# Optimization experiments

Hardware: AMD Instinct MI355X
Metric: run time of the kernel (lower is better)

The kernel has to match this reference:

```python
import jax, jax.numpy as jnp
import numpy as np

R0 = 1.0
N_NODES = 10000
N_EDGES = 160000
DIM_A, DIM_V, DIM_D, CHAN = 64, 32, 16, 16

# Levi-Civita tensor for the antisymmetric (cross-product-like) products
_EPS = np.zeros((3, 3, 3), dtype=np.float32)
for (i, j, k), s in (((0,1,2),1.),((1,2,0),1.),((2,0,1),1.),((0,2,1),-1.),((2,1,0),-1.),((1,0,2),-1.)):
    _EPS[i, j, k] = s


def _tl(W, x):
    """TensLinear: mix channel axis 1 of x (B, din, *(3,)*rank) with W (dout, din)."""
    y = jnp.tensordot(x, W, axes=((1,), (1,)))  # (B, *(3,)*rank, dout)
    return jnp.moveaxis(y, -1, 1)


def radial_encode_8(r, r0):
    # 8 Gaussian radial basis functions on |r|/r0
    d = jnp.linalg.norm(r, axis=-1)            # (E,)
    x = d * (8.0 / r0)
    mu = jnp.arange(8, dtype=r.dtype)
    return jnp.exp(-0.5 * (x[:, None] - mu[None, :]) ** 2)  # (E, 8)


def tens_sigmoid_1(v):
    # equivariant squashing: scale vector by tanh(|v|)/|v|
    n = jnp.linalg.norm(v, axis=-1, keepdims=True)
    return v * jnp.tanh(n) / (n + 1e-12)


def _forward(floats, src, dst, n_nodes):
    (r_ij, x_a, x_v, x_d, W_L0, W_L1, W_L2,
     W_Y000, W_Y110, W_Y220, W_Y011, W_Y101, W_Y121, W_Y211,
     W_Y022, W_Y202, W_Y112, W_Y222, W_Y111, W_Y212,
     W_enc, b_enc, W_dir, W1, b1, W2, b2, W3, b3) = floats
    eps = jnp.asarray(_EPS)
    rad = radial_encode_8(r_ij, R0) @ W_enc.T + b_enc        # (E, chan)
    r = tens_sigmoid_1(r_ij * (7.0 / R0))                    # (E, 3)
    phi_a = rad                                              # (E, chan)
    phi_v = rad[:, :, None] * r[:, None, :]                  # (E, chan, 3)
    phi_d = rad[:, :, None, None] * r[:, None, None, :] * r[:, None, :, None]  # (E, chan, 3, 3)
    # gather destination-node features per edge
    x_a_j = _tl(W_L0, x_a)[dst]                              # (E, chan)
    x_v_j = _tl(W_L1, x_v)[dst]                              # (E, chan, 3)
    x_d_j = _tl(W_L2, x_d)[dst]                              # (E, chan, 3, 3)
    # equivariant tensor products (Bee.apply)
    y_000 = x_a_j * phi_a
    y_110 = jnp.sum(x_v_j * phi_v, -1)
    y_220 = jnp.sum(x_d_j * phi_d, (-2, -1))
    y_011 = x_a_j[..., None] * phi_v
    y_101 = x_v_j * phi_a[..., None]
    y_121 = jnp.einsum('ecj,ecji->eci', x_v_j, phi_d)
    y_211 = jnp.einsum('ecij,ecj->eci', x_d_j, phi_v)
    y_022 = x_a_j[..., None, None] * phi_d
    y_202 = x_d_j * phi_a[..., None, None]
    y_112 = x_v_j[..., :, None] * phi_v[..., None, :]
    y_222 = jnp.einsum('ecik,eckj->ecij', x_d_j, phi_d)
    y_111 = jnp.cross(x_v_j, phi_v)
    y_212 = jnp.einsum('ikl,eckj,ecl->ecij', eps, x_d_j, phi_v)
    psi_a = _tl(W_Y000, y_000) + _tl(W_Y110, y_110) + _tl(W_Y220, y_220)
    psi_v = (_tl(W_Y011, y_011) + _tl(W_Y101, y_101) + _tl(W_Y121, y_121)
             + _tl(W_Y211, y_211) + _tl(W_Y111, y_111))
    psi_d = (_tl(W_Y022, y_022) + _tl(W_Y202, y_202) + _tl(W_Y112, y_112)
             + _tl(W_Y222, y_222) + _tl(W_Y212, y_212))
    # residual MLP on the scalar channel: lin_direct(x) + layers(x)
    lrelu = lambda x: jnp.where(x >= 0, x, 0.1 * x)
    h = lrelu(psi_a @ W1.T + b1)
    h = lrelu(h @ W2.T + b2)
    psi_a = psi_a + psi_a @ W_dir.T + (h @ W3.T + b3)
    # scatter-reduce messages to source nodes
    B_a = jax.ops.segment_sum(psi_a, src, num_segments=n_nodes)
    B_v = jax.ops.segment_sum(psi_v, src, num_segments=n_nodes)
    B_d = jax.ops.segment_sum(psi_d, src, num_segments=n_nodes)
    return 0.1 * B_a, 0.1 * B_v, 0.1 * B_d


def setup_inputs() -> dict:
    key = jax.random.key(0)
    ks = jax.random.split(key, 32)
    f32 = jnp.float32
    nrm = lambda k, shape, scale=1.0: scale * jax.random.normal(k, shape, dtype=f32)
    E, N = N_EDGES, N_NODES
    sC = CHAN ** -0.5
    inp = {
        'r_ij': nrm(ks[0], (E, 3)),
        'x_a': nrm(ks[1], (N, DIM_A)),
        'x_v': nrm(ks[2], (N, DIM_V, 3)),
        'x_d': nrm(ks[3], (N, DIM_D, 3, 3)),
        'W_L0': nrm(ks[4], (CHAN, DIM_A), DIM_A ** -0.5),
        'W_L1': nrm(ks[5], (CHAN, DIM_V), DIM_V ** -0.5),
        'W_L2': nrm(ks[6], (CHAN, DIM_D), DIM_D ** -0.5),
        'W_Y000': nrm(ks[7], (DIM_A, CHAN), sC),
        'W_Y110': nrm(ks[8], (DIM_A, CHAN), sC),
        'W_Y220': nrm(ks[9], (DIM_A, CHAN), sC),
        'W_Y011': nrm(ks[10], (DIM_V, CHAN), sC),
        'W_Y101': nrm(ks[11], (DIM_V, CHAN), sC),
        'W_Y121': nrm(ks[12], (DIM_V, CHAN), sC),
        'W_Y211': nrm(ks[13], (DIM_V, CHAN), sC),
        'W_Y022': nrm(ks[14], (DIM_D, CHAN), sC),
        'W_Y202': nrm(ks[15], (DIM_D, CHAN), sC),
        'W_Y112': nrm(ks[16], (DIM_D, CHAN), sC),
        'W_Y222': nrm(ks[17], (DIM_D, CHAN), sC),
        'W_Y111': nrm(ks[18], (DIM_V, CHAN), sC),
        'W_Y212': nrm(ks[19], (DIM_D, CHAN), sC),
        'W_enc': nrm(ks[20], (CHAN, 8), 8 ** -0.5),
        'b_enc': jnp.zeros((CHAN,), f32),
        'W_dir': nrm(ks[21], (DIM_A, DIM_A), DIM_A ** -0.5),
        'W1': nrm(ks[22], (2 * DIM_A, DIM_A), DIM_A ** -0.5),
        'b1': jnp.zeros((2 * DIM_A,), f32),
        'W2': nrm(ks[23], (2 * DIM_A, 2 * DIM_A), (2 * DIM_A) ** -0.5),
        'b2': jnp.zeros((2 * DIM_A,), f32),
        'W3': nrm(ks[24], (DIM_A, 2 * DIM_A), (2 * DIM_A) ** -0.5),
        'b3': jnp.zeros((DIM_A,), f32),
        'src': jax.random.randint(ks[25], (E,), 0, N, dtype=jnp.int32),
        'dst': jax.random.randint(ks[26], (E,), 0, N, dtype=jnp.int32),
        'n_nodes': N,
    }
    return inp


def reference(r_ij, x_a, x_v, x_d, W_L0, W_L1, W_L2, W_Y000, W_Y110, W_Y220,
              W_Y011, W_Y101, W_Y121, W_Y211, W_Y022, W_Y202, W_Y112, W_Y222,
              W_Y111, W_Y212, W_enc, b_enc, W_dir, W1, b1, W2, b2, W3, b3,
              src, dst, n_nodes):
    floats = (r_ij, x_a, x_v, x_d, W_L0, W_L1, W_L2, W_Y000, W_Y110, W_Y220,
              W_Y011, W_Y101, W_Y121, W_Y211, W_Y022, W_Y202, W_Y112, W_Y222,
              W_Y111, W_Y212, W_enc, b_enc, W_dir, W1, b1, W2, b2, W3, b3)
    return _forward(floats, src, dst, n_nodes)
```

## Files before the change

### kernel.cpp

```cpp
#include <hip/hip_runtime.h>
#include <hip/hip_bf16.h>

typedef __hip_bfloat16 bf16;
typedef __attribute__((ext_vector_type(8))) short bf16x8;
typedef __attribute__((ext_vector_type(4))) float f32x4;

__device__ __forceinline__ void st_bf16(short* p, float v) {
    uint32_t u = __float_as_uint(v) + 0x8000u;
    *p = (short)(u >> 16);
}
__device__ __forceinline__ float bb2f(short s) {
    uint32_t u = ((uint32_t)(uint16_t)s) << 16;
    return __uint_as_float(u);
}

__global__ void zero_i32(int* p, int n) {
    int i = blockIdx.x * blockDim.x + threadIdx.x;
    int stride = gridDim.x * blockDim.x;
    for (; i < n; i += stride) p[i] = 0;
}

__global__ __launch_bounds__(256) void prep_all(
    const float* __restrict__ W000, const float* __restrict__ W110, const float* __restrict__ W220,
    const float* __restrict__ W011, const float* __restrict__ W101, const float* __restrict__ W121,
    const float* __restrict__ W211, const float* __restrict__ W111,
    const float* __restrict__ W022, const float* __restrict__ W202, const float* __restrict__ W112,
    const float* __restrict__ W222, const float* __restrict__ W212,
    const float* __restrict__ W1, const float* __restrict__ W2, const float* __restrict__ W3,
    const float* __restrict__ Wdir, bf16* __restrict__ wout,
    const float* __restrict__ xa, const float* __restrict__ xv, const float* __restrict__ xd,
    const float* __restrict__ WL0, const float* __restrict__ WL1, const float* __restrict__ WL2,
    float* __restrict__ Pa, float* __restrict__ Pv, float* __restrict__ Pd, int N, int NPB,
    const int* __restrict__ src, int* __restrict__ cnt, int E)
{
    int b = blockIdx.x;
    const int tid = threadIdx.x;
    if (b < 178) {
        int i = b * 256 + tid;
        if (i >= 45568) return;
        float v = 0.f;
        if (i < 4096) {
            int o = i >> 6, k = i & 63;
            if (k < 48) {
                int t = k >> 4, c = k & 15;
                const float* W = (t == 0) ? W000 : (t == 1) ? W110 : W220;
                v = W[o * 16 + c];
            }
        } else if (i < 7168) {
            int r = i - 4096, ch = r / 96, k = r % 96;
            if (k < 80) {
                int t = k >> 4, c = k & 15;
                const float* W = (t == 0) ? W011 : (t == 1) ? W101 : (t == 2) ? W121 : (t == 3) ? W211 : W111;
                v = W[ch * 16 + c];
            }
        } else if (i < 8704) {
            int r = i - 7168, ch = r / 96, k = r % 96;
            if (k < 80) {
                int t = k >> 4, c = k & 15;
                const float* W = (t == 0) ? W022 : (t == 1) ? W202 : (t == 2) ? W112 : (t == 3) ? W222 : W212;
                v = W[ch * 16 + c];
            }
        } else if (i < 16896) v = W1[i - 8704];
        else if (i < 33280) v = W2[i - 16896];
        else if (i < 41472) v = W3[i - 33280];
        else v = Wdir[i - 41472];
        wout[i] = __float2bfloat16(v);
        return;
    }
    b -= 178;
    if (b < NPB) {
        __shared__ float sxa[256], sxv[384], sxd[576];
        const int n0 = b * 4;
        if (n0 + tid / 64 < N) sxa[tid] = xa[(size_t)n0 * 64 + tid];
        for (int i = tid; i < 384; i += 256) if (n0 + i / 96 < N)  sxv[i] = xv[(size_t)n0 * 96 + i];
        for (int i = tid; i < 576; i += 256) if (n0 + i / 144 < N) sxd[i] = xd[(size_t)n0 * 144 + i];
        __syncthreads();
        for (int o = tid; o < 832; o += 256) {
            int ln = o / 208, s = o % 208;
            int n = n0 + ln;
            if (n >= N) continue;
            if (s < 16) {
                float a = 0.f;
                const float* w = WL0 + s * 64;
                const float* x = sxa + ln * 64;
                for (int d = 0; d < 64; ++d) a += w[d] * x[d];
                Pa[(size_t)n * 16 + s] = a;
            } else if (s < 64) {
                int idx = s - 16, c = idx / 3, i = idx % 3;
                float a = 0.f;
                const float* w = WL1 + c * 32;
                const float* x = sxv + ln * 96;
                for (int d = 0; d < 32; ++d) a += w[d] * x[d * 3 + i];
                Pv[(size_t)n * 64 + c * 4 + i] = a;
            } else {
                int idx = s - 64, c = idx / 9, ij = idx % 9;
                float a = 0.f;
                const float* w = WL2 + c * 16;
                const float* x = sxd + ln * 144;
                for (int d = 0; d < 16; ++d) a += w[d] * x[d * 9 + ij];
                Pd[(size_t)n * 192 + c * 12 + ij] = a;
            }
        }
        return;
    }
    b -= NPB;
    int i = b * 256 + tid;
    if (i < E) atomicAdd(&cnt[src[i]], 1);
}

__global__ void scan_rows(const int* __restrict__ cnt, int* __restrict__ rowstart, int N) {
    __shared__ int ps[256];
    int t = threadIdx.x;
    int chunk = (N + 255) / 256;
    int base = t * chunk;
    int s = 0;
    for (int i = 0; i < chunk; ++i) { int idx = base + i; if (idx < N) s += cnt[idx]; }
    ps[t] = s;
    __syncthreads();
    for (int off = 1; off < 256; off <<= 1) {
        int v = (t >= off) ? ps[t - off] : 0;
        __syncthreads();
        ps[t] += v;
        __syncthreads();
    }
    int run = (t > 0) ? ps[t - 1] : 0;
    for (int i = 0; i < chunk; ++i) {
        int idx = base + i;
        if (idx < N) { rowstart[idx] = run; run += cnt[idx]; }
    }
    if (t == 255) rowstart[N] = run;
}

__global__ void fill_slot(const int* __restrict__ src, const int* __restrict__ rowstart,
                          int* __restrict__ cursor, int* __restrict__ slot, int E) {
    int i = blockIdx.x * 256 + threadIdx.x;
    if (i < E) slot[i] = rowstart[src[i]] + atomicAdd(&cursor[src[i]], 1);
}

__global__ __launch_bounds__(256) void edge_mfma(
    const float* __restrict__ r_ij,
    const float* __restrict__ Pa, const float* __restrict__ Pv, const float* __restrict__ Pd,
    const float* __restrict__ Wenc, const float* __restrict__ benc,
    const bf16* __restrict__ Wa, const bf16* __restrict__ Wv, const bf16* __restrict__ Wd,
    const bf16* __restrict__ Wb1, const bf16* __restrict__ Wb2,
    const bf16* __restrict__ Wb3, const bf16* __restrict__ Wbdir,
    const float* __restrict__ b1, const float* __restrict__ b2, const float* __restrict__ b3,
    const int* __restrict__ slot, const int* __restrict__ dst,
    short* __restrict__ psi, int E)
{
    __shared__ __align__(16) char smem[32320];
    short* SYA   = (short*)smem;
    short* SYV   = (short*)(smem + 1536);
    short* SYD   = (short*)(smem + 9216);
    int*   SSLOT = (int*)(smem + 32256);
    short* SPSIA = (short*)(smem + 1536);
    short* SH1   = (short*)(smem + 3840);
    short* SH2   = (short*)(smem + 8192);
    short* SPSI  = (short*)(smem + 12544);

    const int tid = threadIdx.x;
    const int e0 = blockIdx.x * 16;
    const bf16x8 z8 = {};

    {
        const int le = tid >> 4, c = tid & 15;
        const int e = e0 + le;
        if (e < E) {
            const int j = dst[e];
            if (c == 0) SSLOT[le] = slot[e];
            float vx = 7.f * r_ij[e * 3 + 0];
            float vy = 7.f * r_ij[e * 3 + 1];
            float vz = 7.f * r_ij[e * 3 + 2];
            float nn = sqrtf(vx * vx + vy * vy + vz * vz);
            float ex = __expf(-2.f * nn);
            float th = (1.f - ex) * __builtin_amdgcn_rcpf(1.f + ex);
            float sc = th * __builtin_amdgcn_rcpf(nn + 1e-12f);
            float rr[3] = {vx * sc, vy * sc, vz * sc};
            float x8 = nn * (8.f / 7.f);
            float rad = benc[c];
            #pragma unroll
            for (int m = 0; m < 8; ++m) {
                float tt = x8 - (float)m;
                rad += __expf(-0.5f * tt * tt) * Wenc[c * 8 + m];
            }
            float xa = Pa[j * 16 + c];
            f32x4 pv4 = *(const f32x4*)(Pv + (size_t)j * 64 + c * 4);
            f32x4 pd0 = *(const f32x4*)(Pd + (size_t)j * 192 + c * 12);
            f32x4 pd1 = *(const f32x4*)(Pd + (size_t)j * 192 + c * 12 + 4);
            f32x4 pd2 = *(const f32x4*)(Pd + (size_t)j * 192 + c * 12 + 8);
            float xv[3] = {pv4[0], pv4[1], pv4[2]};
            float xd[9] = {pd0[0], pd0[1], pd0[2], pd0[3], pd1[0], pd1[1], pd1[2], pd1[3], pd2[0]};
            float dotv = xv[0] * rr[0] + xv[1] * rr[1] + xv[2] * rr[2];
            float mv[3];
            #pragma unroll
            for (int i = 0; i < 3; ++i)
                mv[i] = xd[i * 3] * rr[0] + xd[i * 3 + 1] * rr[1] + xd[i * 3 + 2] * rr[2];
            float quad = mv[0] * rr[0] + mv[1] * rr[1] + mv[2] * rr[2];
            st_bf16(&SYA[le * 48 + c],      xa * rad);
            st_bf16(&SYA[le * 48 + 16 + c], rad * dotv);
            st_bf16(&SYA[le * 48 + 32 + c], rad * quad);
            #pragma unroll
            for (int i = 0; i < 3; ++i) {
                int row = (le * 3 + i) * 80;
                int i1 = (i + 1) % 3, i2 = (i + 2) % 3;
                st_bf16(&SYV[row + c],      xa * rad * rr[i]);
                st_bf16(&SYV[row + 16 + c], rad * xv[i]);
                st_bf16(&SYV[row + 32 + c], rad * dotv * rr[i]);
                st_bf16(&SYV[row + 48 + c], rad * mv[i]);
                st_bf16(&SYV[row + 64 + c], rad * (xv[i1] * rr[i2] - xv[i2] * rr[i1]));
            }
            #pragma unroll
            for (int i = 0; i < 3; ++i) {
                int i1 = (i + 1) % 3, i2 = (i + 2) % 3;
                #pragma unroll
                for (int jj = 0; jj < 3; ++jj) {
                    int row = (le * 9 + i * 3 + jj) * 80;
                    st_bf16(&SYD[row + c],      xa * rad * rr[i] * rr[jj]);
                    st_bf16(&SYD[row + 16 + c], rad * xd[i * 3 + jj]);
                    st_bf16(&SYD[row + 32 + c], rad * xv[i] * rr[jj]);
                    st_bf16(&SYD[row + 48 + c], rad * mv[i] * rr[jj]);
                    st_bf16(&SYD[row + 64 + c], rad * (xd[i1 * 3 + jj] * rr[i2] - xd[i2 * 3 + jj] * rr[i1]));
                }
            }
        }
    }
    __syncthreads();

    const int wid = tid >> 6, lane = tid & 63;
    const int q = lane >> 4, r16 = lane & 15;

    f32x4 da[4] = {};
    f32x4 dv[3][2] = {};
    f32x4 dd[5] = {};
    const int mstart = (wid == 2) ? 0 : 5;
    const int mcnt = (wid == 2) ? 5 : 4;

    if (wid == 0) {
        bf16x8 af0 = *(const bf16x8*)&SYA[r16 * 48 + q * 8];
        bf16x8 af1 = z8;
        if (q < 2) af1 = *(const bf16x8*)&SYA[r16 * 48 + 32 + q * 8];
        #pragma unroll
        for (int n = 0; n < 4; ++n) {
            bf16x8 bf0 = *(const bf16x8*)((const short*)Wa + (n * 16 + r16) * 64 + q * 8);
            bf16x8 bf1 = *(const bf16x8*)((const short*)Wa + (n * 16 + r16) * 64 + 32 + q * 8);
            da[n] = __builtin_amdgcn_mfma_f32_16x16x32_bf16(af0, bf0, da[n], 0, 0, 0);
            da[n] = __builtin_amdgcn_mfma_f32_16x16x32_bf16(af1, bf1, da[n], 0, 0, 0);
        }
    } else if (wid == 1) {
        #pragma unroll
        for (int ks = 0; ks < 3; ++ks) {
            bf16x8 av[3], bv[2];
            #pragma unroll
            for (int m = 0; m < 3; ++m) {
                if (ks < 2) av[m] = *(const bf16x8*)&SYV[(m * 16 + r16) * 80 + ks * 32 + q * 8];
                else {
                    av[m] = z8;
                    if (q < 2) av[m] = *(const bf16x8*)&SYV[(m * 16 + r16) * 80 + 64 + q * 8];
                }
            }
            #pragma unroll
            for (int n = 0; n < 2; ++n)
                bv[n] = *(const bf16x8*)((const short*)Wv + (n * 16 + r16) * 96 + ks * 32 + q * 8);
            #pragma unroll
            for (int m = 0; m < 3; ++m)
                #pragma unroll
                for (int n = 0; n < 2; ++n)
                    dv[m][n] = __builtin_amdgcn_mfma_f32_16x16x32_bf16(av[m], bv[n], dv[m][n], 0, 0, 0);
        }
    } else {
        #pragma unroll
        for (int ks = 0; ks < 3; ++ks) {
            bf16x8 bf = *(const bf16x8*)((const short*)Wd + r16 * 96 + ks * 32 + q * 8);
            for (int mi = 0; mi < mcnt; ++mi) {
                bf16x8 af;
                if (ks < 2) af = *(const bf16x8*)&SYD[((mstart + mi) * 16 + r16) * 80 + ks * 32 + q * 8];
                else {
                    af = z8;
                    if (q < 2) af = *(const bf16x8*)&SYD[((mstart + mi) * 16 + r16) * 80 + 64 + q * 8];
                }
                dd[mi] = __builtin_amdgcn_mfma_f32_16x16x32_bf16(af, bf, dd[mi], 0, 0, 0);
            }
        }
    }
    __syncthreads();

    if (wid == 0) {
        #pragma unroll
        for (int n = 0; n < 4; ++n)
            #pragma unroll
            for (int jj = 0; jj < 4; ++jj)
                st_bf16(&SPSIA[(q * 4 + jj) * 72 + n * 16 + r16], da[n][jj]);
    } else if (wid == 1) {
        #pragma unroll
        for (int m = 0; m < 3; ++m)
            #pragma unroll
            for (int n = 0; n < 2; ++n)
                #pragma unroll
                for (int jj = 0; jj < 4; ++jj) {
                    int row = m * 16 + q * 4 + jj;
                    int el = row / 3, i = row % 3;
                    st_bf16(&SPSI[el * 304 + 64 + (n * 16 + r16) * 3 + i], dv[m][n][jj]);
                }
    } else {
        for (int mi = 0; mi < mcnt; ++mi)
            #pragma unroll
            for (int jj = 0; jj < 4; ++jj) {
                int row = (mstart + mi) * 16 + q * 4 + jj;
                int el = row / 9, ij = row % 9;
                st_bf16(&SPSI[el * 304 + 160 + r16 * 9 + ij], dd[mi][jj]);
            }
    }
    __syncthreads();

    {
        f32x4 h1a[2] = {};
        #pragma unroll
        for (int ks = 0; ks < 2; ++ks) {
            bf16x8 af = *(const bf16x8*)&SPSIA[r16 * 72 + ks * 32 + q * 8];
            #pragma unroll
            for (int n = 0; n < 2; ++n) {
                int col = wid * 32 + n * 16 + r16;
                bf16x8 bf = *(const bf16x8*)((const short*)Wb1 + col * 64 + ks * 32 + q * 8);
                h1a[n] = __builtin_amdgcn_mfma_f32_16x16x32_bf16(af, bf, h1a[n], 0, 0, 0);
            }
        }
        #pragma unroll
        for (int n = 0; n < 2; ++n) {
            int col = wid * 32 + n * 16 + r16;
            float bias = b1[col];
            #pragma unroll
            for (int jj = 0; jj < 4; ++jj) {
                float v = h1a[n][jj] + bias;
                v = v >= 0.f ? v : 0.1f * v;
                st_bf16(&SH1[(q * 4 + jj) * 136 + col], v);
            }
        }
    }
    __syncthreads();
    {
        f32x4 h2a[2] = {};
        #pragma unroll
        for (int ks = 0; ks < 4; ++ks) {
            bf16x8 af = *(const bf16x8*)&SH1[r16 * 136 + ks * 32 + q * 8];
            #pragma unroll
            for (int n = 0; n < 2; ++n) {
                int col = wid * 32 + n * 16 + r16;
                bf16x8 bf = *(const bf16x8*)((const short*)Wb2 + col * 128 + ks * 32 + q * 8);
                h2a[n] = __builtin_amdgcn_mfma_f32_16x16x32_bf16(af, bf, h2a[n], 0, 0, 0);
            }
        }
        #pragma unroll
        for (int n = 0; n < 2; ++n) {
            int col = wid * 32 + n * 16 + r16;
            float bias = b2[col];
            #pragma unroll
            for (int jj = 0; jj < 4; ++jj) {
                float v = h2a[n][jj] + bias;
                v = v >= 0.f ? v : 0.1f * v;
                st_bf16(&SH2[(q * 4 + jj) * 136 + col], v);
            }
        }
    }
    __syncthreads();
    {
        f32x4 o3 = {};
        const int col3 = wid * 16 + r16;
        #pragma unroll
        for (int ks = 0; ks < 4; ++ks) {
            bf16x8 af = *(const bf16x8*)&SH2[r16 * 136 + ks * 32 + q * 8];
            bf16x8 bf = *(const bf16x8*)((const short*)Wb3 + col3 * 128 + ks * 32 + q * 8);
            o3 = __builtin_amdgcn_mfma_f32_16x16x32_bf16(af, bf, o3, 0, 0, 0);
        }
        #pragma unroll
        for (int ks = 0; ks < 2; ++ks) {
            bf16x8 af = *(const bf16x8*)&SPSIA[r16 * 72 + ks * 32 + q * 8];
            bf16x8 bf = *(const bf16x8*)((const short*)Wbdir + col3 * 64 + ks * 32 + q * 8);
            o3 = __builtin_amdgcn_mfma_f32_16x16x32_bf16(af, bf, o3, 0, 0, 0);
        }
        float bias = b3[col3];
        #pragma unroll
        for (int jj = 0; jj < 4; ++jj) {
            int row = q * 4 + jj;
            float v = o3[jj] + bias + bb2f(SPSIA[row * 72 + col3]);
            st_bf16(&SPSI[row * 304 + col3], v);
        }
    }
    __syncthreads();

    {
        const uint32_t* S32 = (const uint32_t*)SPSI;
        uint32_t* P32 = (uint32_t*)psi;
        for (int idx = tid; idx < 16 * 152; idx += 256) {
            int le = idx / 152, k = idx - le * 152;
            if (e0 + le < E)
                P32[(size_t)SSLOT[le] * 152 + k] = S32[le * 152 + k];
        }
    }
}

__global__ __launch_bounds__(192) void gather(
    const short* __restrict__ psi, const int* __restrict__ rowstart,
    float* __restrict__ out, int N) {
    int n = blockIdx.x, t = threadIdx.x;
    if (t >= 152) return;
    int s0 = rowstart[n], s1 = rowstart[n + 1];
    const uint32_t* p32 = (const uint32_t*)psi;
    float a0 = 0.f, a1 = 0.f;
    for (int s = s0; s < s1; ++s) {
        uint32_t u = p32[(size_t)s * 152 + t];
        a0 += __uint_as_float(u << 16);
        a1 += __uint_as_float(u & 0xffff0000u);
    }
    int f = 2 * t;
    float2 v = make_float2(0.1f * a0, 0.1f * a1);
    if (f < 64)       *(float2*)&out[(size_t)n * 64 + f] = v;
    else if (f < 160) *(float2*)&out[(size_t)N * 64 + (size_t)n * 96 + (f - 64)] = v;
    else              *(float2*)&out[(size_t)N * 160 + (size_t)n * 144 + (f - 160)] = v;
}

extern "C" void kernel_launch(void* const* d_in, const int* in_sizes, int n_in,
                              void* d_out, int out_size, void* d_ws, size_t ws_size,
                              hipStream_t stream) {
    const float* r_ij = (const float*)d_in[0];
    const float* x_a  = (const float*)d_in[1];
    const float* x_v  = (const float*)d_in[2];
    const float* x_d  = (const float*)d_in[3];
    const float* W_L0 = (const float*)d_in[4];
    const float* W_L1 = (const float*)d_in[5];
    const float* W_L2 = (const float*)d_in[6];
    const float* W000 = (const float*)d_in[7];
    const float* W110 = (const float*)d_in[8];
    const float* W220 = (const float*)d_in[9];
    const float* W011 = (const float*)d_in[10];
    const float* W101 = (const float*)d_in[11];
    const float* W121 = (const float*)d_in[12];
    const float* W211 = (const float*)d_in[13];
    const float* W022 = (const float*)d_in[14];
    const float* W202 = (const float*)d_in[15];
    const float* W112 = (const float*)d_in[16];
    const float* W222 = (const float*)d_in[17];
    const float* W111 = (const float*)d_in[18];
    const float* W212 = (const float*)d_in[19];
    const float* Wenc = (const float*)d_in[20];
    const float* benc = (const float*)d_in[21];
    const float* Wdir = (const float*)d_in[22];
    const float* W1   = (const float*)d_in[23];
    const float* b1   = (const float*)d_in[24];
    const float* W2   = (const float*)d_in[25];
    const float* b2   = (const float*)d_in[26];
    const float* W3   = (const float*)d_in[27];
    const float* b3   = (const float*)d_in[28];
    const int* src    = (const int*)d_in[29];
    const int* dst    = (const int*)d_in[30];

    const int E = in_sizes[29];
    const int N = in_sizes[1] / 64;

    float* Pa     = (float*)d_ws;
    float* Pv     = Pa + (size_t)N * 16;
    float* Pd     = Pv + (size_t)N * 64;
    bf16*  Wb     = (bf16*)(Pd + (size_t)N * 192);
    int*   cnt    = (int*)(Wb + 45568);
    int*   cursor = cnt + N;
    int*   rowst  = cursor + N;
    int*   slot   = rowst + N + 1;
    short* psi    = (short*)(slot + E);

    const bf16* Wa_p    = Wb;
    const bf16* Wv_p    = Wb + 4096;
    const bf16* Wd_p    = Wb + 7168;
    const bf16* Wb1_p   = Wb + 8704;
    const bf16* Wb2_p   = Wb + 16896;
    const bf16* Wb3_p   = Wb + 33280;
    const bf16* Wbdir_p = Wb + 41472;

    const int NPB = (N + 3) / 4;
    const int HB  = (E + 255) / 256;

    zero_i32<<<80, 256, 0, stream>>>(cnt, 2 * N);
    prep_all<<<178 + NPB + HB, 256, 0, stream>>>(
        W000, W110, W220, W011, W101, W121, W211, W111,
        W022, W202, W112, W222, W212, W1, W2, W3, Wdir, Wb,
        x_a, x_v, x_d, W_L0, W_L1, W_L2, Pa, Pv, Pd, N, NPB,
        src, cnt, E);
    scan_rows<<<1, 256, 0, stream>>>(cnt, rowst, N);
    fill_slot<<<HB, 256, 0, stream>>>(src, rowst, cursor, slot, E);
    edge_mfma<<<(E + 15) / 16, 256, 0, stream>>>(
        r_ij, Pa, Pv, Pd, Wenc, benc,
        Wa_p, Wv_p, Wd_p, Wb1_p, Wb2_p, Wb3_p, Wbdir_p,
        b1, b2, b3, slot, dst, psi, E);
    gather<<<N, 192, 0, stream>>>(psi, rowst, (float*)d_out, N);
}
```

Baseline: 242.1 us.

## Sort edges by destination with XCD-aware tile mapping for cache locality

Builds a second CSR keyed on dst and processes edges in dst-sorted order in edge_mfma, so that gathered node features (Pa/Pv/Pd) are reused by neighbouring edges. The block index is remapped so each XCD handles a contiguous run of tiles, which keeps the reused node data in that XCD's L2. The gather kernel now reads two words per thread with 128-thread blocks, and the zero kernel is replaced by a memset. The cost is extra atomics, a second scan and an indirection load through eperm.

```diff
diff --git a/kernel.cpp b/kernel.cpp
--- a/kernel.cpp
+++ b/kernel.cpp
@@ -12,12 +12,6 @@
 __device__ __forceinline__ float bb2f(short s) {
     uint32_t u = ((uint32_t)(uint16_t)s) << 16;
     return __uint_as_float(u);
-}
-
-__global__ void zero_i32(int* p, int n) {
-    int i = blockIdx.x * blockDim.x + threadIdx.x;
-    int stride = gridDim.x * blockDim.x;
-    for (; i < n; i += stride) p[i] = 0;
 }
 
 __global__ __launch_bounds__(256) void prep_all(
@@ -31,7 +25,8 @@
     const float* __restrict__ xa, const float* __restrict__ xv, const float* __restrict__ xd,
     const float* __restrict__ WL0, const float* __restrict__ WL1, const float* __restrict__ WL2,
     float* __restrict__ Pa, float* __restrict__ Pv, float* __restrict__ Pd, int N, int NPB,
-    const int* __restrict__ src, int* __restrict__ cnt, int E)
+    const int* __restrict__ src, const int* __restrict__ dst,
+    int* __restrict__ cnt_s, int* __restrict__ cnt_d, int E)
 {
     int b = blockIdx.x;
     const int tid = threadIdx.x;
@@ -105,10 +100,16 @@
     }
     b -= NPB;
     int i = b * 256 + tid;
-    if (i < E) atomicAdd(&cnt[src[i]], 1);
-}
-
-__global__ void scan_rows(const int* __restrict__ cnt, int* __restrict__ rowstart, int N) {
+    if (i < E) {
+        atomicAdd(&cnt_s[src[i]], 1);
+        atomicAdd(&cnt_d[dst[i]], 1);
+    }
+}
+
+__global__ void scan_rows2(const int* __restrict__ cnt_s, int* __restrict__ rs_s,
+                           const int* __restrict__ cnt_d, int* __restrict__ rs_d, int N) {
+    const int* cnt = blockIdx.x ? cnt_d : cnt_s;
+    int* rowstart = blockIdx.x ? rs_d : rs_s;
     __shared__ int ps[256];
     int t = threadIdx.x;
     int chunk = (N + 255) / 256;
@@ -131,10 +132,16 @@
     if (t == 255) rowstart[N] = run;
 }
 
-__global__ void fill_slot(const int* __restrict__ src, const int* __restrict__ rowstart,
-                          int* __restrict__ cursor, int* __restrict__ slot, int E) {
+__global__ void fill_slot(const int* __restrict__ src, const int* __restrict__ dst,
+                          const int* __restrict__ rs_s, const int* __restrict__ rs_d,
+                          int* __restrict__ cur_s, int* __restrict__ cur_d,
+                          int* __restrict__ slot, int* __restrict__ eperm, int E) {
     int i = blockIdx.x * 256 + threadIdx.x;
-    if (i < E) slot[i] = rowstart[src[i]] + atomicAdd(&cursor[src[i]], 1);
+    if (i < E) {
+        slot[i] = rs_s[src[i]] + atomicAdd(&cur_s[src[i]], 1);
+        int p = rs_d[dst[i]] + atomicAdd(&cur_d[dst[i]], 1);
+        eperm[p] = i;
+    }
 }
 
 __global__ __launch_bounds__(256) void edge_mfma(
@@ -146,7 +153,8 @@
     const bf16* __restrict__ Wb3, const bf16* __restrict__ Wbdir,
     const float* __restrict__ b1, const float* __restrict__ b2, const float* __restrict__ b3,
     const int* __restrict__ slot, const int* __restrict__ dst,
-    short* __restrict__ psi, int E)
+    const int* __restrict__ eperm,
+    short* __restrict__ psi, int E, int nwg)
 {
     __shared__ __align__(16) char smem[32320];
     short* SYA   = (short*)smem;
@@ -159,13 +167,17 @@
     short* SPSI  = (short*)(smem + 12544);
 
     const int tid = threadIdx.x;
-    const int e0 = blockIdx.x * 16;
+    int orig = blockIdx.x;
+    int q = nwg >> 3, r = nwg & 7;
+    int xcd = orig & 7, idx = orig >> 3;
+    int tile = (xcd < r) ? (xcd * (q + 1) + idx) : (r * (q + 1) + (xcd - r) * q + idx);
+    const int e0 = tile * 16;
     const bf16x8 z8 = {};
 
     {
         const int le = tid >> 4, c = tid & 15;
-        const int e = e0 + le;
-        if (e < E) {
+        if (e0 + le < E) {
+            const int e = eperm[e0 + le];
             const int j = dst[e];
             if (c == 0) SSLOT[le] = slot[e];
             float vx = 7.f * r_ij[e * 3 + 0];
@@ -227,7 +239,7 @@
     __syncthreads();
 
     const int wid = tid >> 6, lane = tid & 63;
-    const int q = lane >> 4, r16 = lane & 15;
+    const int q16 = lane >> 4, r16 = lane & 15;
 
     f32x4 da[4] = {};
     f32x4 dv[3][2] = {};
@@ -236,13 +248,13 @@
     const int mcnt = (wid == 2) ? 5 : 4;
 
     if (wid == 0) {
-        bf16x8 af0 = *(const bf16x8*)&SYA[r16 * 48 + q * 8];
+        bf16x8 af0 = *(const bf16x8*)&SYA[r16 * 48 + q16 * 8];
         bf16x8 af1 = z8;
-        if (q < 2) af1 = *(const bf16x8*)&SYA[r16 * 48 + 32 + q * 8];
+        if (q16 < 2) af1 = *(const bf16x8*)&SYA[r16 * 48 + 32 + q16 * 8];
         #pragma unroll
         for (int n = 0; n < 4; ++n) {
-            bf16x8 bf0 = *(const bf16x8*)((const short*)Wa + (n * 16 + r16) * 64 + q * 8);
-            bf16x8 bf1 = *(const bf16x8*)((const short*)Wa + (n * 16 + r16) * 64 + 32 + q * 8);
+            bf16x8 bf0 = *(const bf16x8*)((const short*)Wa + (n * 16 + r16) * 64 + q16 * 8);
+            bf16x8 bf1 = *(const bf16x8*)((const short*)Wa + (n * 16 + r16) * 64 + 32 + q16 * 8);
             da[n] = __builtin_amdgcn_mfma_f32_16x16x32_bf16(af0, bf0, da[n], 0, 0, 0);
             da[n] = __builtin_amdgcn_mfma_f32_16x16x32_bf16(af1, bf1, da[n], 0, 0, 0);
         }
@@ -252,15 +264,15 @@
             bf16x8 av[3], bv[2];
             #pragma unroll
             for (int m = 0; m < 3; ++m) {
-                if (ks < 2) av[m] = *(const bf16x8*)&SYV[(m * 16 + r16) * 80 + ks * 32 + q * 8];
+                if (ks < 2) av[m] = *(const bf16x8*)&SYV[(m * 16 + r16) * 80 + ks * 32 + q16 * 8];
                 else {
                     av[m] = z8;
-                    if (q < 2) av[m] = *(const bf16x8*)&SYV[(m * 16 + r16) * 80 + 64 + q * 8];
+                    if (q16 < 2) av[m] = *(const bf16x8*)&SYV[(m * 16 + r16) * 80 + 64 + q16 * 8];
                 }
             }
             #pragma unroll
             for (int n = 0; n < 2; ++n)
-                bv[n] = *(const bf16x8*)((const short*)Wv + (n * 16 + r16) * 96 + ks * 32 + q * 8);
+                bv[n] = *(const bf16x8*)((const short*)Wv + (n * 16 + r16) * 96 + ks * 32 + q16 * 8);
             #pragma unroll
             for (int m = 0; m < 3; ++m)
                 #pragma unroll
@@ -270,13 +282,13 @@
     } else {
         #pragma unroll
         for (int ks = 0; ks < 3; ++ks) {
-            bf16x8 bf = *(const bf16x8*)((const short*)Wd + r16 * 96 + ks * 32 + q * 8);
+            bf16x8 bf = *(const bf16x8*)((const short*)Wd + r16 * 96 + ks * 32 + q16 * 8);
             for (int mi = 0; mi < mcnt; ++mi) {
                 bf16x8 af;
-                if (ks < 2) af = *(const bf16x8*)&SYD[((mstart + mi) * 16 + r16) * 80 + ks * 32 + q * 8];
+                if (ks < 2) af = *(const bf16x8*)&SYD[((mstart + mi) * 16 + r16) * 80 + ks * 32 + q16 * 8];
                 else {
                     af = z8;
-                    if (q < 2) af = *(const bf16x8*)&SYD[((mstart + mi) * 16 + r16) * 80 + 64 + q * 8];
+                    if (q16 < 2) af = *(const bf16x8*)&SYD[((mstart + mi) * 16 + r16) * 80 + 64 + q16 * 8];
                 }
                 dd[mi] = __builtin_amdgcn_mfma_f32_16x16x32_bf16(af, bf, dd[mi], 0, 0, 0);
             }
@@ -289,7 +301,7 @@
         for (int n = 0; n < 4; ++n)
             #pragma unroll
             for (int jj = 0; jj < 4; ++jj)
-                st_bf16(&SPSIA[(q * 4 + jj) * 72 + n * 16 + r16], da[n][jj]);
+                st_bf16(&SPSIA[(q16 * 4 + jj) * 72 + n * 16 + r16], da[n][jj]);
     } else if (wid == 1) {
         #pragma unroll
         for (int m = 0; m < 3; ++m)
@@ -297,7 +309,7 @@
             for (int n = 0; n < 2; ++n)
                 #pragma unroll
                 for (int jj = 0; jj < 4; ++jj) {
-                    int row = m * 16 + q * 4 + jj;
+                    int row = m * 16 + q16 * 4 + jj;
                     int el = row / 3, i = row % 3;
                     st_bf16(&SPSI[el * 304 + 64 + (n * 16 + r16) * 3 + i], dv[m][n][jj]);
                 }
@@ -305,7 +317,7 @@
         for (int mi = 0; mi < mcnt; ++mi)
             #pragma unroll
             for (int jj = 0; jj < 4; ++jj) {
-                int row = (mstart + mi) * 16 + q * 4 + jj;
+                int row = (mstart + mi) * 16 + q16 * 4 + jj;
                 int el = row / 9, ij = row % 9;
                 st_bf16(&SPSI[el * 304 + 160 + r16 * 9 + ij], dd[mi][jj]);
             }
@@ -316,11 +328,11 @@
         f32x4 h1a[2] = {};
         #pragma unroll
         for (int ks = 0; ks < 2; ++ks) {
-            bf16x8 af = *(const bf16x8*)&SPSIA[r16 * 72 + ks * 32 + q * 8];
+            bf16x8 af = *(const bf16x8*)&SPSIA[r16 * 72 + ks * 32 + q16 * 8];
             #pragma unroll
             for (int n = 0; n < 2; ++n) {
                 int col = wid * 32 + n * 16 + r16;
-                bf16x8 bf = *(const bf16x8*)((const short*)Wb1 + col * 64 + ks * 32 + q * 8);
+                bf16x8 bf = *(const bf16x8*)((const short*)Wb1 + col * 64 + ks * 32 + q16 * 8);
                 h1a[n] = __builtin_amdgcn_mfma_f32_16x16x32_bf16(af, bf, h1a[n], 0, 0, 0);
             }
         }
@@ -332,7 +344,7 @@
             for (int jj = 0; jj < 4; ++jj) {
                 float v = h1a[n][jj] + bias;
                 v = v >= 0.f ? v : 0.1f * v;
-                st_bf16(&SH1[(q * 4 + jj) * 136 + col], v);
+                st_bf16(&SH1[(q16 * 4 + jj) * 136 + col], v);
             }
         }
     }
@@ -341,11 +353,11 @@
         f32x4 h2a[2] = {};
         #pragma unroll
         for (int ks = 0; ks < 4; ++ks) {
-            bf16x8 af = *(const bf16x8*)&SH1[r16 * 136 + ks * 32 + q * 8];
+            bf16x8 af = *(const bf16x8*)&SH1[r16 * 136 + ks * 32 + q16 * 8];
             #pragma unroll
             for (int n = 0; n < 2; ++n) {
                 int col = wid * 32 + n * 16 + r16;
-                bf16x8 bf = *(const bf16x8*)((const short*)Wb2 + col * 128 + ks * 32 + q * 8);
+                bf16x8 bf = *(const bf16x8*)((const short*)Wb2 + col * 128 + ks * 32 + q16 * 8);
                 h2a[n] = __builtin_amdgcn_mfma_f32_16x16x32_bf16(af, bf, h2a[n], 0, 0, 0);
             }
         }
@@ -357,7 +369,7 @@
             for (int jj = 0; jj < 4; ++jj) {
                 float v = h2a[n][jj] + bias;
                 v = v >= 0.f ? v : 0.1f * v;
-                st_bf16(&SH2[(q * 4 + jj) * 136 + col], v);
+                st_bf16(&SH2[(q16 * 4 + jj) * 136 + col], v);
             }
         }
     }
@@ -367,20 +379,20 @@
         const int col3 = wid * 16 + r16;
         #pragma unroll
         for (int ks = 0; ks < 4; ++ks) {
-            bf16x8 af = *(const bf16x8*)&SH2[r16 * 136 + ks * 32 + q * 8];
-            bf16x8 bf = *(const bf16x8*)((const short*)Wb3 + col3 * 128 + ks * 32 + q * 8);
+            bf16x8 af = *(const bf16x8*)&SH2[r16 * 136 + ks * 32 + q16 * 8];
+            bf16x8 bf = *(const bf16x8*)((const short*)Wb3 + col3 * 128 + ks * 32 + q16 * 8);
             o3 = __builtin_amdgcn_mfma_f32_16x16x32_bf16(af, bf, o3, 0, 0, 0);
         }
         #pragma unroll
         for (int ks = 0; ks < 2; ++ks) {
-            bf16x8 af = *(const bf16x8*)&SPSIA[r16 * 72 + ks * 32 + q * 8];
-            bf16x8 bf = *(const bf16x8*)((const short*)Wbdir + col3 * 64 + ks * 32 + q * 8);
+            bf16x8 af = *(const bf16x8*)&SPSIA[r16 * 72 + ks * 32 + q16 * 8];
+            bf16x8 bf = *(const bf16x8*)((const short*)Wbdir + col3 * 64 + ks * 32 + q16 * 8);
             o3 = __builtin_amdgcn_mfma_f32_16x16x32_bf16(af, bf, o3, 0, 0, 0);
         }
         float bias = b3[col3];
         #pragma unroll
         for (int jj = 0; jj < 4; ++jj) {
-            int row = q * 4 + jj;
+            int row = q16 * 4 + jj;
             float v = o3[jj] + bias + bb2f(SPSIA[row * 72 + col3]);
             st_bf16(&SPSI[row * 304 + col3], v);
         }
@@ -390,32 +402,34 @@
     {
         const uint32_t* S32 = (const uint32_t*)SPSI;
         uint32_t* P32 = (uint32_t*)psi;
-        for (int idx = tid; idx < 16 * 152; idx += 256) {
-            int le = idx / 152, k = idx - le * 152;
+        for (int idx2 = tid; idx2 < 16 * 152; idx2 += 256) {
+            int le = idx2 / 152, k = idx2 - le * 152;
             if (e0 + le < E)
                 P32[(size_t)SSLOT[le] * 152 + k] = S32[le * 152 + k];
         }
     }
 }
 
-__global__ __launch_bounds__(192) void gather(
+__global__ __launch_bounds__(128) void gather(
     const short* __restrict__ psi, const int* __restrict__ rowstart,
     float* __restrict__ out, int N) {
     int n = blockIdx.x, t = threadIdx.x;
-    if (t >= 152) return;
+    if (t >= 76) return;
     int s0 = rowstart[n], s1 = rowstart[n + 1];
-    const uint32_t* p32 = (const uint32_t*)psi;
-    float a0 = 0.f, a1 = 0.f;
+    float a0 = 0.f, a1 = 0.f, a2 = 0.f, a3 = 0.f;
     for (int s = s0; s < s1; ++s) {
-        uint32_t u = p32[(size_t)s * 152 + t];
-        a0 += __uint_as_float(u << 16);
-        a1 += __uint_as_float(u & 0xffff0000u);
-    }
-    int f = 2 * t;
-    float2 v = make_float2(0.1f * a0, 0.1f * a1);
-    if (f < 64)       *(float2*)&out[(size_t)n * 64 + f] = v;
-    else if (f < 160) *(float2*)&out[(size_t)N * 64 + (size_t)n * 96 + (f - 64)] = v;
-    else              *(float2*)&out[(size_t)N * 160 + (size_t)n * 144 + (f - 160)] = v;
+        const uint32_t* p = (const uint32_t*)(psi + (size_t)s * 304) + 2 * t;
+        uint32_t u0 = p[0], u1 = p[1];
+        a0 += __uint_as_float(u0 << 16);
+        a1 += __uint_as_float(u0 & 0xffff0000u);
+        a2 += __uint_as_float(u1 << 16);
+        a3 += __uint_as_float(u1 & 0xffff0000u);
+    }
+    int f = 4 * t;
+    f32x4 v = {0.1f * a0, 0.1f * a1, 0.1f * a2, 0.1f * a3};
+    if (f < 64)       *(f32x4*)&out[(size_t)n * 64 + f] = v;
+    else if (f < 160) *(f32x4*)&out[(size_t)N * 64 + (size_t)n * 96 + (f - 64)] = v;
+    else              *(f32x4*)&out[(size_t)N * 160 + (size_t)n * 144 + (f - 160)] = v;
 }
 
 extern "C" void kernel_launch(void* const* d_in, const int* in_sizes, int n_in,
@@ -460,11 +474,15 @@
     float* Pv     = Pa + (size_t)N * 16;
     float* Pd     = Pv + (size_t)N * 64;
     bf16*  Wb     = (bf16*)(Pd + (size_t)N * 192);
-    int*   cnt    = (int*)(Wb + 45568);
-    int*   cursor = cnt + N;
-    int*   rowst  = cursor + N;
-    int*   slot   = rowst + N + 1;
-    short* psi    = (short*)(slot + E);
+    int*   cnt_s  = (int*)(Wb + 45568);
+    int*   cur_s  = cnt_s + N;
+    int*   cnt_d  = cur_s + N;
+    int*   cur_d  = cnt_d + N;
+    int*   rs_s   = cur_d + N;
+    int*   rs_d   = rs_s + N + 1;
+    int*   slot   = rs_d + N + 1;
+    int*   eperm  = slot + E;
+    short* psi    = (short*)(eperm + E);
 
     const bf16* Wa_p    = Wb;
     const bf16* Wv_p    = Wb + 4096;
@@ -476,18 +494,19 @@
 
     const int NPB = (N + 3) / 4;
     const int HB  = (E + 255) / 256;
-
-    zero_i32<<<80, 256, 0, stream>>>(cnt, 2 * N);
+    const int nwg = (E + 15) / 16;
+
+    hipMemsetAsync(cnt_s, 0, (size_t)4 * N * sizeof(int), stream);
     prep_all<<<178 + NPB + HB, 256, 0, stream>>>(
         W000, W110, W220, W011, W101, W121, W211, W111,
         W022, W202, W112, W222, W212, W1, W2, W3, Wdir, Wb,
         x_a, x_v, x_d, W_L0, W_L1, W_L2, Pa, Pv, Pd, N, NPB,
-        src, cnt, E);
-    scan_rows<<<1, 256, 0, stream>>>(cnt, rowst, N);
-    fill_slot<<<HB, 256, 0, stream>>>(src, rowst, cursor, slot, E);
-    edge_mfma<<<(E + 15) / 16, 256, 0, stream>>>(
+        src, dst, cnt_s, cnt_d, E);
+    scan_rows2<<<2, 256, 0, stream>>>(cnt_s, rs_s, cnt_d, rs_d, N);
+    fill_slot<<<HB, 256, 0, stream>>>(src, dst, rs_s, rs_d, cur_s, cur_d, slot, eperm, E);
+    edge_mfma<<<nwg, 256, 0, stream>>>(
         r_ij, Pa, Pv, Pd, Wenc, benc,
         Wa_p, Wv_p, Wd_p, Wb1_p, Wb2_p, Wb3_p, Wbdir_p,
-        b1, b2, b3, slot, dst, psi, E);
-    gather<<<N, 192, 0, stream>>>(psi, rowst, (float*)d_out, N);
-}
+        b1, b2, b3, slot, dst, eperm, psi, E, nwg);
+    gather<<<N, 128, 0, stream>>>(psi, rs_s, (float*)d_out, N);
+}
```

Result: slower. 253.9 us (+4.9%).
